# Kernel optimization log

Measured on AMD Instinct MI355X. Metric: run time of the kernel, lower is better.

## Reference

```python
import jax, jax.numpy as jnp
import numpy as np

IN_CH = 128
EMBED = 64
ALPHA = 0.2  # leaky relu slope
NEG_INF = jnp.float32(-9e15)


def setup_inputs() -> dict:
    key = jax.random.key(0)
    k_x, k_adj, k_W, k_a, k_b = jax.random.split(key, 5)
    B, N = 2, 512
    x = jax.random.normal(k_x, (B, N, IN_CH), dtype=jnp.float32)
    adj = jax.random.randint(k_adj, (B, N, N), 0, 2, dtype=jnp.int32)
    # xavier_uniform with gain=1.414
    gain = 1.414
    lim_W = gain * np.sqrt(6.0 / (IN_CH + EMBED))
    W = jax.random.uniform(k_W, (IN_CH, EMBED), jnp.float32, -lim_W, lim_W)
    lim_a = gain * np.sqrt(6.0 / (2 * EMBED + 1))
    a = jax.random.uniform(k_a, (2 * EMBED, 1), jnp.float32, -lim_a, lim_a)
    bias = jax.random.normal(k_b, (EMBED,), dtype=jnp.float32) * 0.02
    return {"x": x, "adj": adj, "W": W, "a": a, "bias": bias}


def reference(x, adj, W, a, bias):
    B, N, _ = x.shape
    D = W.shape[1]
    hidden = jnp.matmul(x, W)                      # [B, N, D]
    # Faithful reproduction of the original's repeat_interleave/repeat + cat(dim=1) + view.
    chunks = jnp.repeat(hidden, N, axis=1)         # [B, N*N, D]
    alt = jnp.tile(hidden, (1, N, 1))              # [B, N*N, D]
    allc = jnp.concatenate([chunks, alt], axis=1).reshape(B, N, N, 2 * D)
    attn = jnp.matmul(allc, a)[..., 0]             # [B, N, N]
    attn = jnp.where(attn >= 0, attn, ALPHA * attn)  # leaky relu
    attn = jnp.where(adj > 0, attn, NEG_INF)
    attention = jax.nn.softmax(attn, axis=-1)
    # dropout omitted: reference is eval-mode (deterministic)
    out = jnp.matmul(attention, hidden) + bias     # [B, N, D]
    return out
```

## Files before the change

kernel.cpp:

```cpp
#include <hip/hip_runtime.h>
#include <math.h>

#define GN 512
#define GB 2
#define INCH 128
#define GD 64
#define ALPHA 0.2f
#define NEG_INF_F (-9e15f)

__global__ __launch_bounds__(64) void k_hidden(
        const float* __restrict__ x, const float* __restrict__ W,
        const float* __restrict__ a,
        float* __restrict__ hidden, float* __restrict__ s1,
        float* __restrict__ s2, float* __restrict__ s12) {
    const int row = blockIdx.x;
    const int d = threadIdx.x;
    __shared__ float xs[INCH];
    const float* xr = x + (size_t)row * INCH;
    xs[d] = xr[d];
    xs[d + 64] = xr[d + 64];
    __syncthreads();
    float h = 0.f;
    #pragma unroll
    for (int k = 0; k < INCH; ++k) h = fmaf(xs[k], W[k * GD + d], h);
    hidden[(size_t)row * GD + d] = h;
    float p1 = a[d] * h;
    float p2 = a[GD + d] * h;
    #pragma unroll
    for (int off = 32; off > 0; off >>= 1) {
        p1 += __shfl_down(p1, off, 64);
        p2 += __shfl_down(p2, off, 64);
    }
    if (d == 0) { s1[row] = p1; s2[row] = p2; s12[row] = p1 + p2; }
}

__global__ __launch_bounds__(256) void k_attn(
        const int* __restrict__ adj, const float* __restrict__ hidden,
        const float* __restrict__ s1, const float* __restrict__ s2,
        const float* __restrict__ s12, const float* __restrict__ bias,
        float* __restrict__ out) {
    const int blk = blockIdx.x;
    const int b = blk >> 9;
    const int i = blk & (GN - 1);
    const int tid = threadIdx.x;
    const int lane = tid & 63;
    const int wave = tid >> 6;

    __shared__ float p[GN];
    __shared__ float red[8];
    __shared__ float acc[4][GD];

    const int* adjrow = adj + ((size_t)b * GN + i) * GN;
    const float* s1b  = s1  + b * GN;
    const float* s2b  = s2  + b * GN;
    const float* s12b = s12 + b * GN;

    float v[2];
    #pragma unroll
    for (int t = 0; t < 2; ++t) {
        const int j = tid + t * 256;
        float pre;
        if (i < 256) {
            pre = s12b[2 * i + (j >= 256 ? 1 : 0)];
        } else {
            const int m = j & 255;
            pre = s1b[2 * m] + s2b[2 * m + 1];
        }
        pre = (pre >= 0.f) ? pre : ALPHA * pre;
        v[t] = (adjrow[j] > 0) ? pre : NEG_INF_F;
    }

    float mx = fmaxf(v[0], v[1]);
    #pragma unroll
    for (int off = 32; off > 0; off >>= 1) mx = fmaxf(mx, __shfl_xor(mx, off, 64));
    if (lane == 0) red[wave] = mx;
    __syncthreads();
    mx = fmaxf(fmaxf(red[0], red[1]), fmaxf(red[2], red[3]));

    const float e0 = expf(v[0] - mx);
    const float e1 = expf(v[1] - mx);
    p[tid] = e0;
    p[tid + 256] = e1;
    float s = e0 + e1;
    #pragma unroll
    for (int off = 32; off > 0; off >>= 1) s += __shfl_xor(s, off, 64);
    if (lane == 0) red[4 + wave] = s;
    __syncthreads();
    const float inv = 1.f / (red[4] + red[5] + red[6] + red[7]);

    const int d = tid & 63;
    const int c = wave;
    const float* hb = hidden + (size_t)b * GN * GD;
    float av = 0.f;
    const int j0 = c * 128;
    #pragma unroll 8
    for (int j = j0; j < j0 + 128; ++j)
        av = fmaf(p[j], hb[(size_t)j * GD + d], av);
    acc[c][d] = av;
    __syncthreads();
    if (tid < GD) {
        const float o = (acc[0][tid] + acc[1][tid] + acc[2][tid] + acc[3][tid]) * inv
                        + bias[tid];
        out[((size_t)b * GN + i) * GD + tid] = o;
    }
}

extern "C" void kernel_launch(void* const* d_in, const int* in_sizes, int n_in,
                              void* d_out, int out_size, void* d_ws, size_t ws_size,
                              hipStream_t stream) {
    const float* x    = (const float*)d_in[0];
    const int*   adj  = (const int*)d_in[1];
    const float* W    = (const float*)d_in[2];
    const float* a    = (const float*)d_in[3];
    const float* bias = (const float*)d_in[4];
    float* out = (float*)d_out;

    float* ws     = (float*)d_ws;
    float* hidden = ws;
    float* s1     = hidden + GB * GN * GD;
    float* s2     = s1 + GB * GN;
    float* s12    = s2 + GB * GN;

    k_hidden<<<GB * GN, 64, 0, stream>>>(x, W, a, hidden, s1, s2, s12);
    k_attn<<<GB * GN, 256, 0, stream>>>(adj, hidden, s1, s2, s12, bias, out);
}
```

Baseline: 17.17 us.

## Process four attention rows per block and stage W in shared memory

The attention kernel now handles four query rows per 512-thread block. One wave computes each row's masked softmax, and all eight waves then share each hidden load across four row accumulators. This cuts reloads of the hidden matrix and the number of blocks. The hidden-projection kernel now computes four rows per block with W copied into 32KB of LDS. Both changes raise per-block LDS use and use fewer blocks (256 and 256 instead of 1024), which could reduce parallelism on a large GPU.

```diff
diff --git a/kernel.cpp b/kernel.cpp
--- a/kernel.cpp
+++ b/kernel.cpp
@@ -7,101 +7,137 @@
 #define GD 64
 #define ALPHA 0.2f
 #define NEG_INF_F (-9e15f)
+#define TI 4
 
-__global__ __launch_bounds__(64) void k_hidden(
+__global__ __launch_bounds__(256) void k_hidden(
         const float* __restrict__ x, const float* __restrict__ W,
         const float* __restrict__ a,
         float* __restrict__ hidden, float* __restrict__ s1,
         float* __restrict__ s2, float* __restrict__ s12) {
-    const int row = blockIdx.x;
-    const int d = threadIdx.x;
-    __shared__ float xs[INCH];
-    const float* xr = x + (size_t)row * INCH;
-    xs[d] = xr[d];
-    xs[d + 64] = xr[d + 64];
+    const int row0 = blockIdx.x * 4;
+    const int tid = threadIdx.x;
+    __shared__ float Wl[INCH * GD];
+    __shared__ float xs[4][INCH];
+
+    const float4* W4 = (const float4*)W;
+    float4* Wl4 = (float4*)Wl;
+    #pragma unroll
+    for (int idx = tid; idx < INCH * GD / 4; idx += 256) Wl4[idx] = W4[idx];
+    const float4* x4 = (const float4*)(x + (size_t)row0 * INCH);
+    if (tid < 4 * INCH / 4) ((float4*)xs)[tid] = x4[tid];
     __syncthreads();
+
+    const int r = tid >> 6, d = tid & 63;
     float h = 0.f;
     #pragma unroll
-    for (int k = 0; k < INCH; ++k) h = fmaf(xs[k], W[k * GD + d], h);
-    hidden[(size_t)row * GD + d] = h;
-    float p1 = a[d] * h;
-    float p2 = a[GD + d] * h;
+    for (int k = 0; k < INCH; ++k) h = fmaf(xs[r][k], Wl[k * GD + d], h);
+    hidden[(size_t)(row0 + r) * GD + d] = h;
+
+    float p1 = a[d] * h, p2 = a[GD + d] * h;
     #pragma unroll
     for (int off = 32; off > 0; off >>= 1) {
-        p1 += __shfl_down(p1, off, 64);
-        p2 += __shfl_down(p2, off, 64);
+        p1 += __shfl_xor(p1, off, 64);
+        p2 += __shfl_xor(p2, off, 64);
     }
-    if (d == 0) { s1[row] = p1; s2[row] = p2; s12[row] = p1 + p2; }
+    if (d == 0) { s1[row0 + r] = p1; s2[row0 + r] = p2; s12[row0 + r] = p1 + p2; }
 }
 
-__global__ __launch_bounds__(256) void k_attn(
+__global__ __launch_bounds__(512) void k_attn(
         const int* __restrict__ adj, const float* __restrict__ hidden,
         const float* __restrict__ s1, const float* __restrict__ s2,
         const float* __restrict__ s12, const float* __restrict__ bias,
         float* __restrict__ out) {
     const int blk = blockIdx.x;
-    const int b = blk >> 9;
-    const int i = blk & (GN - 1);
+    const int b = blk >> 7;
+    const int i0 = (blk & 127) * TI;
     const int tid = threadIdx.x;
     const int lane = tid & 63;
-    const int wave = tid >> 6;
+    const int w = tid >> 6;
 
-    __shared__ float p[GN];
-    __shared__ float red[8];
-    __shared__ float acc[4][GD];
+    __shared__ float pl[TI][GN];
+    __shared__ float red[8][TI][GD];
+    __shared__ float invs[TI];
 
-    const int* adjrow = adj + ((size_t)b * GN + i) * GN;
     const float* s1b  = s1  + b * GN;
     const float* s2b  = s2  + b * GN;
     const float* s12b = s12 + b * GN;
 
-    float v[2];
-    #pragma unroll
-    for (int t = 0; t < 2; ++t) {
-        const int j = tid + t * 256;
-        float pre;
+    if (w < TI) {
+        const int i = i0 + w;
+        const int* adjrow = adj + ((size_t)b * GN + i) * GN;
+        float v[8];
         if (i < 256) {
-            pre = s12b[2 * i + (j >= 256 ? 1 : 0)];
+            float c0 = s12b[2 * i], c1 = s12b[2 * i + 1];
+            c0 = c0 >= 0.f ? c0 : ALPHA * c0;
+            c1 = c1 >= 0.f ? c1 : ALPHA * c1;
+            #pragma unroll
+            for (int seg = 0; seg < 8; ++seg) {
+                const int j = seg * 64 + lane;
+                v[seg] = adjrow[j] > 0 ? (seg < 4 ? c0 : c1) : NEG_INF_F;
+            }
         } else {
-            const int m = j & 255;
-            pre = s1b[2 * m] + s2b[2 * m + 1];
+            #pragma unroll
+            for (int seg = 0; seg < 8; ++seg) {
+                const int j = seg * 64 + lane;
+                const int m = j & 255;
+                float pre = s1b[2 * m] + s2b[2 * m + 1];
+                pre = pre >= 0.f ? pre : ALPHA * pre;
+                v[seg] = adjrow[j] > 0 ? pre : NEG_INF_F;
+            }
         }
-        pre = (pre >= 0.f) ? pre : ALPHA * pre;
-        v[t] = (adjrow[j] > 0) ? pre : NEG_INF_F;
+        float mx = v[0];
+        #pragma unroll
+        for (int seg = 1; seg < 8; ++seg) mx = fmaxf(mx, v[seg]);
+        #pragma unroll
+        for (int off = 32; off > 0; off >>= 1) mx = fmaxf(mx, __shfl_xor(mx, off, 64));
+        float s = 0.f;
+        #pragma unroll
+        for (int seg = 0; seg < 8; ++seg) {
+            const float e = expf(v[seg] - mx);
+            pl[w][seg * 64 + lane] = e;
+            s += e;
+        }
+        #pragma unroll
+        for (int off = 32; off > 0; off >>= 1) s += __shfl_xor(s, off, 64);
+        if (lane == 0) invs[w] = 1.f / s;
     }
+    __syncthreads();
 
-    float mx = fmaxf(v[0], v[1]);
-    #pragma unroll
-    for (int off = 32; off > 0; off >>= 1) mx = fmaxf(mx, __shfl_xor(mx, off, 64));
-    if (lane == 0) red[wave] = mx;
+    const float* hb = hidden + (size_t)b * GN * GD;
+    const int j0 = w * 64;
+    float acc0 = 0.f, acc1 = 0.f, acc2 = 0.f, acc3 = 0.f;
+    #pragma unroll 4
+    for (int jj = 0; jj < 64; jj += 4) {
+        const int j = j0 + jj;
+        const float4 q0 = *(const float4*)&pl[0][j];
+        const float4 q1 = *(const float4*)&pl[1][j];
+        const float4 q2 = *(const float4*)&pl[2][j];
+        const float4 q3 = *(const float4*)&pl[3][j];
+        float hv;
+        hv = hb[(size_t)(j + 0) * GD + lane];
+        acc0 = fmaf(q0.x, hv, acc0); acc1 = fmaf(q1.x, hv, acc1);
+        acc2 = fmaf(q2.x, hv, acc2); acc3 = fmaf(q3.x, hv, acc3);
+        hv = hb[(size_t)(j + 1) * GD + lane];
+        acc0 = fmaf(q0.y, hv, acc0); acc1 = fmaf(q1.y, hv, acc1);
+        acc2 = fmaf(q2.y, hv, acc2); acc3 = fmaf(q3.y, hv, acc3);
+        hv = hb[(size_t)(j + 2) * GD + lane];
+        acc0 = fmaf(q0.z, hv, acc0); acc1 = fmaf(q1.z, hv, acc1);
+        acc2 = fmaf(q2.z, hv, acc2); acc3 = fmaf(q3.z, hv, acc3);
+        hv = hb[(size_t)(j + 3) * GD + lane];
+        acc0 = fmaf(q0.w, hv, acc0); acc1 = fmaf(q1.w, hv, acc1);
+        acc2 = fmaf(q2.w, hv, acc2); acc3 = fmaf(q3.w, hv, acc3);
+    }
+    red[w][0][lane] = acc0; red[w][1][lane] = acc1;
+    red[w][2][lane] = acc2; red[w][3][lane] = acc3;
     __syncthreads();
-    mx = fmaxf(fmaxf(red[0], red[1]), fmaxf(red[2], red[3]));
 
-    const float e0 = expf(v[0] - mx);
-    const float e1 = expf(v[1] - mx);
-    p[tid] = e0;
-    p[tid + 256] = e1;
-    float s = e0 + e1;
-    #pragma unroll
-    for (int off = 32; off > 0; off >>= 1) s += __shfl_xor(s, off, 64);
-    if (lane == 0) red[4 + wave] = s;
-    __syncthreads();
-    const float inv = 1.f / (red[4] + red[5] + red[6] + red[7]);
-
-    const int d = tid & 63;
-    const int c = wave;
-    const float* hb = hidden + (size_t)b * GN * GD;
-    float av = 0.f;
-    const int j0 = c * 128;
-    #pragma unroll 8
-    for (int j = j0; j < j0 + 128; ++j)
-        av = fmaf(p[j], hb[(size_t)j * GD + d], av);
-    acc[c][d] = av;
-    __syncthreads();
-    if (tid < GD) {
-        const float o = (acc[0][tid] + acc[1][tid] + acc[2][tid] + acc[3][tid]) * inv
-                        + bias[tid];
-        out[((size_t)b * GN + i) * GD + tid] = o;
+    if (tid < TI * GD) {
+        const int r = tid >> 6, d = tid & 63;
+        float o = 0.f;
+        #pragma unroll
+        for (int ww = 0; ww < 8; ++ww) o += red[ww][r][d];
+        o = o * invs[r] + bias[d];
+        out[((size_t)b * GN + i0 + r) * GD + d] = o;
     }
 }
 
@@ -117,10 +153,10 @@
 
     float* ws     = (float*)d_ws;
     float* hidden = ws;
-    float* s1     = hidden + GB * GN * GD;
-    float* s2     = s1 + GB * GN;
-    float* s12    = s2 + GB * GN;
+    float* s1f    = hidden + GB * GN * GD;
+    float* s2f    = s1f + GB * GN;
+    float* s12f   = s2f + GB * GN;
 
-    k_hidden<<<GB * GN, 64, 0, stream>>>(x, W, a, hidden, s1, s2, s12);
-    k_attn<<<GB * GN, 256, 0, stream>>>(adj, hidden, s1, s2, s12, bias, out);
+    k_hidden<<<GB * GN / 4, 256, 0, stream>>>(x, W, a, hidden, s1f, s2f, s12f);
+    k_attn<<<GB * GN / TI, 512, 0, stream>>>(adj, hidden, s1f, s2f, s12f, bias, out);
 }
```

After: 15.92 us. 7.3% less time.
